# Kernel tuning notes

Hardware: AMD Instinct MI355X
Metric: run time of the kernel (lower is better)

Reference implementation:

```python
import jax, jax.numpy as jnp
import numpy as np

B, IN, HID, OUT = 1024, 512, 128, 64
INP1 = IN + 1  # 513, after prepending ones column


def setup_inputs() -> dict:
    key = jax.random.key(0)
    k1, k2, k3, k4, k5, k6, k7, k8 = jax.random.split(key, 8)
    s1 = 1.0 / np.sqrt(INP1 * INP1)
    s2 = 1.0 / np.sqrt(HID)
    return {
        "img": jax.random.normal(k1, (B, IN), dtype=jnp.float32),
        "tab": jax.random.normal(k2, (B, IN), dtype=jnp.float32),
        "W1": jax.random.uniform(k3, (HID, INP1 * INP1), jnp.float32, -s1, s1),
        "b1": jax.random.uniform(k4, (HID,), jnp.float32, -s1, s1),
        "W2": jax.random.uniform(k5, (HID, HID), jnp.float32, -s2, s2),
        "b2": jax.random.uniform(k6, (HID,), jnp.float32, -s2, s2),
        "W3": jax.random.uniform(k7, (OUT, HID), jnp.float32, -s2, s2),
        "b3": jax.random.uniform(k8, (OUT,), jnp.float32, -s2, s2),
    }


def reference(img, tab, W1, b1, W2, b2, W3, b3):
    ones = jnp.ones((img.shape[0], 1), dtype=img.dtype)
    x = jnp.concatenate([ones, img], axis=1)  # [B, IN+1]
    t = jnp.concatenate([ones, tab], axis=1)  # [B, IN+1]
    # batched outer product, flattened: [B, (IN+1)*(IN+1)]
    fusion = jnp.einsum("bi,bj->bij", x, t).reshape(x.shape[0], -1)
    # dropout is identity in eval mode
    y1 = fusion @ W1.T + b1
    y2 = jnp.tanh(y1 @ W2.T + b2)
    y3 = jax.nn.relu(y2 @ W3.T + b3)
    return y3
```

## Files before the change

### kernel.cpp

```cpp
#include <hip/hip_runtime.h>
#include <hip/hip_bf16.h>

typedef __bf16 bf16x8 __attribute__((ext_vector_type(8)));
typedef float f32x4 __attribute__((ext_vector_type(4)));
typedef float f32x4u __attribute__((ext_vector_type(4), aligned(4)));
typedef unsigned short u16x8 __attribute__((ext_vector_type(8)));

typedef __attribute__((address_space(1))) const unsigned int gu32;
typedef __attribute__((address_space(3))) unsigned int lu32;

#define B_SZ   1024
#define IN_SZ  512
#define HID    128
#define OUT_SZ 64
#define BK     32
#define NKT    16
#define M2     65536

static __device__ __forceinline__ unsigned short f2bf(float f) {
    __hip_bfloat16 h = __float2bfloat16(f);
    return *reinterpret_cast<unsigned short*>(&h);
}

__global__ __launch_bounds__(256) void prep_kernel(
    const float* __restrict__ img, const float* __restrict__ tab,
    unsigned short* __restrict__ tbt, float* __restrict__ xhT,
    float* __restrict__ tc, const float* __restrict__ w1,
    float* __restrict__ wrowT)
{
    const int blk = blockIdx.x;
    for (int j = threadIdx.x; j < 512; j += 256) {
        float v = (j == 0) ? 1.0f : tab[(size_t)blk * IN_SZ + (j - 1)];
        tbt[(size_t)blk * 512 + j] = f2bf(v);
    }
    if (threadIdx.x == 0) tc[blk] = tab[(size_t)blk * IN_SZ + 511];
    if (blk < 513) {
        for (int b = threadIdx.x; b < B_SZ; b += 256)
            xhT[(size_t)blk * B_SZ + b] =
                (blk == 0) ? 1.0f : img[(size_t)b * IN_SZ + (blk - 1)];
    }
    if (blk < 257) {
        const int idx = blk * 256 + threadIdx.x;
        if (idx < 513 * 128) {
            const int j = idx >> 7, h = idx & 127;
            wrowT[idx] = w1[((size_t)h * 513 + 512) * 513 + j];
        }
    }
}

__global__ __launch_bounds__(512, 4) void gemm_fused(
    const float* __restrict__ w1, const unsigned short* __restrict__ tbt,
    const float* __restrict__ xhT, const float* __restrict__ tc,
    float* __restrict__ y1acc)
{
    __shared__ unsigned short Als[3][128 * BK];
    __shared__ unsigned short Bls[3][256 * BK];

    const int wgid = (blockIdx.x & 7) * 256 + (blockIdx.x >> 3);
    const int bm = wgid >> 2;
    const int bn = wgid & 3;
    const int n0 = bn * 256;
    const int h0    = bm >> 2;
    const int ibase = (bm & 3) * 128;
    const int tid  = threadIdx.x;
    const int wv   = tid >> 6;
    const int wr   = wv >> 2;
    const int wc   = wv & 3;
    const int lane = tid & 63;
    const int l15  = lane & 15;
    const int kg   = lane >> 4;

    const int ar  = tid >> 2;
    const int acl = (tid & 3) ^ ((ar >> 1) & 3);
    const float* asrcF = w1 + ((size_t)h0 * 513 + ibase + ar) * 513 + acl * 8;

    const unsigned short* bsrc[2];
    int bBase[2];
    #pragma unroll
    for (int q = 0; q < 2; ++q) {
        const int p  = q * 512 + tid;
        const int r  = p >> 2;
        const int cl = (p & 3) ^ ((r >> 1) & 3);
        bsrc[q] = tbt + (size_t)(n0 + r) * 512 + cl * 8;
        bBase[q] = (q * 512 + wv * 64) * 8;
    }

    int aoffs[4], boffs[4];
    #pragma unroll
    for (int ms = 0; ms < 4; ++ms) {
        const int r = wr * 64 + ms * 16 + l15;
        aoffs[ms] = (r * 4 + (kg ^ ((r >> 1) & 3))) * 8;
    }
    #pragma unroll
    for (int ns = 0; ns < 4; ++ns) {
        const int r = wc * 64 + ns * 16 + l15;
        boffs[ns] = (r * 4 + (kg ^ ((r >> 1) & 3))) * 8;
    }

    f32x4 acc[4][4] = {};
    f32x4u rAlo, rAhi;

#define STB(BUF, KT) do {                                                    \
        const int k32_ = (KT) * BK;                                          \
        _Pragma("unroll")                                                    \
        for (int q_ = 0; q_ < 2; ++q_)                                       \
            __builtin_amdgcn_global_load_lds(                                \
                (gu32*)(const void*)(bsrc[q_] + k32_),                       \
                (lu32*)(void*)&Bls[BUF][bBase[q_]], 16, 0, 0);               \
    } while (0)
#define CVW8(DST, LO, HI) do {                                               \
        u16x8 u_;                                                            \
        u_[0] = f2bf((LO)[0]); u_[1] = f2bf((LO)[1]);                        \
        u_[2] = f2bf((LO)[2]); u_[3] = f2bf((LO)[3]);                        \
        u_[4] = f2bf((HI)[0]); u_[5] = f2bf((HI)[1]);                        \
        u_[6] = f2bf((HI)[2]); u_[7] = f2bf((HI)[3]);                        \
        *reinterpret_cast<u16x8*>(DST) = u_;                                 \
    } while (0)

    {
        const f32x4u t0lo = *reinterpret_cast<const f32x4u*>(asrcF);
        const f32x4u t0hi = *reinterpret_cast<const f32x4u*>(asrcF + 4);
        const f32x4u t1lo = *reinterpret_cast<const f32x4u*>(asrcF + 32);
        const f32x4u t1hi = *reinterpret_cast<const f32x4u*>(asrcF + 36);
        CVW8(&Als[0][tid * 8], t0lo, t0hi);
        CVW8(&Als[1][tid * 8], t1lo, t1hi);
        STB(0, 0);
        STB(1, 1);
    }
    __syncthreads();

    #pragma unroll
    for (int kt = 0; kt < NKT; ++kt) {
        const int cur = kt % 3;
        const unsigned short* ab = &Als[cur][0];
        const unsigned short* bb = &Bls[cur][0];

        if (kt >= 1 && kt + 1 < NKT)
            CVW8(&Als[(kt + 1) % 3][tid * 8], rAlo, rAhi);
        if (kt + 2 < NKT) {
            const float* s_ = asrcF + (kt + 2) * 32;
            rAlo = *reinterpret_cast<const f32x4u*>(s_);
            rAhi = *reinterpret_cast<const f32x4u*>(s_ + 4);
        }

        bf16x8 af[4];
        #pragma unroll
        for (int ms = 0; ms < 4; ++ms)
            af[ms] = *reinterpret_cast<const bf16x8*>(&ab[aoffs[ms]]);
        __builtin_amdgcn_s_setprio(1);
        #pragma unroll
        for (int ns = 0; ns < 4; ++ns) {
            const bf16x8 bf = *reinterpret_cast<const bf16x8*>(&bb[boffs[ns]]);
            #pragma unroll
            for (int ms = 0; ms < 4; ++ms)
                acc[ms][ns] = __builtin_amdgcn_mfma_f32_16x16x32_bf16(
                    af[ms], bf, acc[ms][ns], 0, 0, 0);
        }
        __builtin_amdgcn_s_setprio(0);

        if (kt == NKT - 1) break;

        if (kt + 2 >= NKT) asm volatile("s_waitcnt vmcnt(0)" ::: "memory");
        else               asm volatile("s_waitcnt vmcnt(2)" ::: "memory");
        if (kt + 2 < NKT) STB((kt + 2) % 3, kt + 2);
        asm volatile("s_waitcnt lgkmcnt(0)" ::: "memory");
        __builtin_amdgcn_s_barrier();
        __builtin_amdgcn_sched_barrier(0);
    }
#undef STB
#undef CVW8

    const size_t orow = (size_t)h0 * 513;
    float wcv[4][4];
    #pragma unroll
    for (int ms = 0; ms < 4; ++ms)
        #pragma unroll
        for (int v = 0; v < 4; ++v) {
            const int i_ = ibase + wr * 64 + ms * 16 + kg * 4 + v;
            wcv[ms][v] = w1[(orow + i_) * 513 + 512];
        }

    #pragma unroll
    for (int ns = 0; ns < 4; ++ns) {
        const int ncol = n0 + wc * 64 + ns * 16 + l15;
        const float tv = tc[ncol];
        float s0 = 0.f;
        #pragma unroll
        for (int ms = 0; ms < 4; ++ms) {
            const int i_ = ibase + wr * 64 + ms * 16 + kg * 4;
            #pragma unroll
            for (int v = 0; v < 4; ++v)
                s0 += (acc[ms][ns][v] + wcv[ms][v] * tv)
                      * xhT[(size_t)(i_ + v) * B_SZ + ncol];
        }
        s0 += __shfl_xor(s0, 16); s0 += __shfl_xor(s0, 32);
        if (lane < 16) atomicAdd(&y1acc[(size_t)ncol * HID + h0], s0);
    }
}

__global__ __launch_bounds__(128) void tailmlp_kernel(
    const float* __restrict__ img, const float* __restrict__ tab,
    const float* __restrict__ wrowT, const float* __restrict__ y1acc,
    const float* __restrict__ b1,
    const float* __restrict__ W2, const float* __restrict__ b2,
    const float* __restrict__ W3, const float* __restrict__ b3,
    float* __restrict__ out)
{
    __shared__ float tls[4][513];
    __shared__ float W2p[128][129];
    __shared__ float W3p[64][129];
    __shared__ float y1ls[4][128];
    __shared__ float y2ls[4][128];

    const int b0 = blockIdx.x * 4;
    const int h  = threadIdx.x;

    #pragma unroll
    for (int g = 0; g < 128; ++g) {
        const int idx = g * 128 + h;
        W2p[idx >> 7][idx & 127] = W2[idx];
    }
    #pragma unroll
    for (int g = 0; g < 64; ++g) {
        const int idx = g * 128 + h;
        W3p[idx >> 7][idx & 127] = W3[idx];
    }
    #pragma unroll
    for (int q = 0; q < 4; ++q)
        for (int j = h; j < 513; j += 128)
            tls[q][j] = (j == 0) ? 1.0f : tab[(size_t)(b0 + q) * IN_SZ + (j - 1)];
    __syncthreads();

    {
        float a0 = 0.f, a1 = 0.f, a2 = 0.f, a3 = 0.f;
        #pragma unroll 8
        for (int j = 0; j < 513; ++j) {
            const float w = wrowT[j * 128 + h];
            a0 += w * tls[0][j]; a1 += w * tls[1][j];
            a2 += w * tls[2][j]; a3 += w * tls[3][j];
        }
        const float bb = b1[h];
        y1ls[0][h] = y1acc[(size_t)(b0 + 0) * HID + h] + bb
                     + a0 * img[(size_t)(b0 + 0) * IN_SZ + 511];
        y1ls[1][h] = y1acc[(size_t)(b0 + 1) * HID + h] + bb
                     + a1 * img[(size_t)(b0 + 1) * IN_SZ + 511];
        y1ls[2][h] = y1acc[(size_t)(b0 + 2) * HID + h] + bb
                     + a2 * img[(size_t)(b0 + 2) * IN_SZ + 511];
        y1ls[3][h] = y1acc[(size_t)(b0 + 3) * HID + h] + bb
                     + a3 * img[(size_t)(b0 + 3) * IN_SZ + 511];
    }
    __syncthreads();

    {
        const float bb = b2[h];
        float s[4] = {bb, bb, bb, bb};
        #pragma unroll 16
        for (int k = 0; k < HID; ++k) {
            const float w = W2p[h][k];
            s[0] += w * y1ls[0][k]; s[1] += w * y1ls[1][k];
            s[2] += w * y1ls[2][k]; s[3] += w * y1ls[3][k];
        }
        #pragma unroll
        for (int q = 0; q < 4; ++q) y2ls[q][h] = tanhf(s[q]);
    }
    __syncthreads();

    if (h < OUT_SZ) {
        const float bb = b3[h];
        float s[4] = {bb, bb, bb, bb};
        #pragma unroll 16
        for (int k = 0; k < HID; ++k) {
            const float w = W3p[h][k];
            s[0] += w * y2ls[0][k]; s[1] += w * y2ls[1][k];
            s[2] += w * y2ls[2][k]; s[3] += w * y2ls[3][k];
        }
        #pragma unroll
        for (int q = 0; q < 4; ++q)
            out[(size_t)(b0 + q) * OUT_SZ + h] = fmaxf(s[q], 0.f);
    }
}

__global__ __launch_bounds__(512, 4) void gemm_fused_fb(
    const float* __restrict__ w1, const unsigned short* __restrict__ tbt,
    const float* __restrict__ xhT, const float* __restrict__ tc,
    float* __restrict__ y1acc)
{
    __shared__ float          Afs[2][64 * BK];
    __shared__ unsigned short Bls[2][512 * BK];

    const int bm = blockIdx.x >> 1;
    const int bn = blockIdx.x & 1;
    const int m0 = bm * 64;
    const int n0 = bn * 512;
    const int tid  = threadIdx.x;
    const int wv   = tid >> 6;
    const int lane = tid & 63;
    const int l15  = lane & 15;
    const int kg   = lane >> 4;

    const int ar  = tid >> 3;
    const int acl = (tid & 7) ^ (ar & 7);
    const float* asrc = w1 + (size_t)(m0 + ar) * 513 + acl * 4;
    const int aBase = (wv * 64) * 4;

    const unsigned short* bsrc[4];
    int bBase[4];
    #pragma unroll
    for (int q = 0; q < 4; ++q) {
        const int p  = q * 512 + tid;
        const int r  = p >> 2;
        const int cl = (p & 3) ^ ((r >> 1) & 3);
        bsrc[q] = tbt + (size_t)(n0 + r) * 512 + cl * 8;
        bBase[q] = (q * 512 + wv * 64) * 8;
    }

    int aoff0[4], aoff1[4], boffs[4];
    #pragma unroll
    for (int ms = 0; ms < 4; ++ms) {
        const int r = ms * 16 + l15;
        aoff0[ms] = r * 32 + (((kg * 2) + 0) ^ (r & 7)) * 4;
        aoff1[ms] = r * 32 + (((kg * 2) + 1) ^ (r & 7)) * 4;
    }
    #pragma unroll
    for (int ns = 0; ns < 4; ++ns) {
        const int r = wv * 64 + ns * 16 + l15;
        boffs[ns] = ((r << 2) | (kg ^ ((r >> 1) & 3))) * 8;
    }

    f32x4 acc[4][4] = {};

#define STAGE_FB(BUF, KT) do {                                               \
        const int k32_ = (KT) * BK;                                          \
        _Pragma("unroll")                                                    \
        for (int q_ = 0; q_ < 4; ++q_)                                       \
            __builtin_amdgcn_global_load_lds(                                \
                (gu32*)(const void*)(bsrc[q_] + k32_),                       \
                (lu32*)(void*)&Bls[BUF][bBase[q_]], 16, 0, 0);               \
        __builtin_amdgcn_global_load_lds(                                    \
            (gu32*)(const void*)(asrc + k32_),                               \
            (lu32*)(void*)&Afs[BUF][aBase], 16, 0, 0);                       \
    } while (0)

    STAGE_FB(0, 0);
    __syncthreads();

    for (int kt = 0; kt < NKT; ++kt) {
        const int cur = kt & 1;
        if (kt + 1 < NKT) STAGE_FB(cur ^ 1, kt + 1);

        const float*          ab = &Afs[cur][0];
        const unsigned short* bb = &Bls[cur][0];
        bf16x8 bfr[4];
        #pragma unroll
        for (int ns = 0; ns < 4; ++ns)
            bfr[ns] = *reinterpret_cast<const bf16x8*>(&bb[boffs[ns]]);
        #pragma unroll
        for (int ms = 0; ms < 4; ++ms) {
            const f32x4 lo = *reinterpret_cast<const f32x4*>(&ab[aoff0[ms]]);
            const f32x4 hi = *reinterpret_cast<const f32x4*>(&ab[aoff1[ms]]);
            u16x8 u;
            u[0] = f2bf(lo[0]); u[1] = f2bf(lo[1]);
            u[2] = f2bf(lo[2]); u[3] = f2bf(lo[3]);
            u[4] = f2bf(hi[0]); u[5] = f2bf(hi[1]);
            u[6] = f2bf(hi[2]); u[7] = f2bf(hi[3]);
            const bf16x8 af = __builtin_bit_cast(bf16x8, u);
            #pragma unroll
            for (int ns = 0; ns < 4; ++ns)
                acc[ms][ns] = __builtin_amdgcn_mfma_f32_16x16x32_bf16(
                    af, bfr[ns], acc[ms][ns], 0, 0, 0);
        }
        __syncthreads();
    }
#undef STAGE_FB

    const int h0 = m0 / 513;
    const int mb = (h0 + 1) * 513;
    const bool cross = (mb < m0 + 64);

    float wcv[4][4];
    #pragma unroll
    for (int ms = 0; ms < 4; ++ms)
        #pragma unroll
        for (int v = 0; v < 4; ++v)
            wcv[ms][v] = w1[(size_t)(m0 + ms * 16 + kg * 4 + v) * 513 + 512];

    #pragma unroll
    for (int ns = 0; ns < 4; ++ns) {
        const int ncol = n0 + wv * 64 + ns * 16 + l15;
        const float tv = tc[ncol];
        float s0 = 0.f, s1 = 0.f;
        #pragma unroll
        for (int ms = 0; ms < 4; ++ms) {
            #pragma unroll
            for (int v = 0; v < 4; ++v) {
                const int m = m0 + ms * 16 + kg * 4 + v;
                const bool lo = (m < mb);
                const int i = lo ? (m - h0 * 513) : (m - mb);
                const float val = (acc[ms][ns][v] + wcv[ms][v] * tv)
                                  * xhT[(size_t)i * B_SZ + ncol];
                if (lo) s0 += val; else s1 += val;
            }
        }
        s0 += __shfl_xor(s0, 16); s0 += __shfl_xor(s0, 32);
        if (lane < 16) atomicAdd(&y1acc[(size_t)ncol * HID + h0], s0);
        if (cross) {
            s1 += __shfl_xor(s1, 16); s1 += __shfl_xor(s1, 32);
            if (lane < 16 && (h0 + 1) < HID)
                atomicAdd(&y1acc[(size_t)ncol * HID + h0 + 1], s1);
        }
    }
}

__global__ __launch_bounds__(128) void mlp_kernel(
    const float* __restrict__ y1acc, const float* __restrict__ b1,
    const float* __restrict__ W2, const float* __restrict__ b2,
    const float* __restrict__ W3, const float* __restrict__ b3,
    float* __restrict__ out)
{
    __shared__ float y1r[HID];
    __shared__ float y2r[HID];
    const int b = blockIdx.x;
    const int h = threadIdx.x;
    y1r[h] = y1acc[(size_t)b * HID + h] + b1[h];
    __syncthreads();
    float a = b2[h];
    const float* w2r = W2 + (size_t)h * HID;
    #pragma unroll 8
    for (int k = 0; k < HID; ++k) a += w2r[k] * y1r[k];
    y2r[h] = tanhf(a);
    __syncthreads();
    if (h < OUT_SZ) {
        float a3 = b3[h];
        const float* w3r = W3 + (size_t)h * HID;
        #pragma unroll 8
        for (int k = 0; k < HID; ++k) a3 += w3r[k] * y2r[k];
        out[(size_t)b * OUT_SZ + h] = fmaxf(a3, 0.f);
    }
}

extern "C" void kernel_launch(void* const* d_in, const int* in_sizes, int n_in,
                              void* d_out, int out_size, void* d_ws, size_t ws_size,
                              hipStream_t stream) {
    const float* img = (const float*)d_in[0];
    const float* tab = (const float*)d_in[1];
    const float* W1  = (const float*)d_in[2];
    const float* b1  = (const float*)d_in[3];
    const float* W2  = (const float*)d_in[4];
    const float* b2  = (const float*)d_in[5];
    const float* W3  = (const float*)d_in[6];
    const float* b3  = (const float*)d_in[7];
    float* out = (float*)d_out;

    char* ws = (char*)d_ws;
    float*          y1acc = (float*)ws;
    unsigned short* tbt   = (unsigned short*)(ws + 524288);
    float*          xhT   = (float*)(ws + 1572864);
    float*          tc    = (float*)(ws + 3674112);
    float*          wrowT = (float*)(ws + 3678208);
    const size_t need = 3678208ULL + 262656ULL;

    hipMemsetAsync(y1acc, 0, (size_t)B_SZ * HID * sizeof(float), stream);
    prep_kernel<<<dim3(1024), dim3(256), 0, stream>>>(img, tab, tbt, xhT, tc,
                                                      W1, wrowT);
    if (ws_size >= need) {
        gemm_fused<<<dim3(2048), dim3(512), 0, stream>>>(W1, tbt, xhT, tc, y1acc);
        tailmlp_kernel<<<dim3(256), dim3(128), 0, stream>>>(
            img, tab, wrowT, y1acc, b1, W2, b2, W3, b3, out);
    } else {
        gemm_fused_fb<<<dim3(2052), dim3(512), 0, stream>>>(W1, tbt, xhT, tc, y1acc);
        mlp_kernel<<<dim3(1024), dim3(128), 0, stream>>>(y1acc, b1, W2, b2, W3, b3, out);
    }
}
```

Baseline: 186.4 us.

## Pre-convert W1 to bf16 in prep pass and stream both GEMM operands via LDS DMA

The prep kernel now converts the main block of W1 to a packed bf16 buffer in the workspace. The GEMM then loads both A and B tiles with global_load_lds instead of doing in-loop fp32 loads, bf16 conversion and LDS stores. The GEMM tile shrinks to 128x128 with 256 threads, and the pipeline waits and barriers at the top of each iteration. The aim is to take the conversion and register staging off the MFMA critical path. In exchange there is an extra full pass over W1 that writes a 64 MB intermediate, and the new path needs a much larger workspace, otherwise the fallback runs.

```diff
diff --git a/kernel.cpp b/kernel.cpp
--- a/kernel.cpp
+++ b/kernel.cpp
@@ -24,16 +24,32 @@
 
 __global__ __launch_bounds__(256) void prep_kernel(
     const float* __restrict__ img, const float* __restrict__ tab,
+    const float* __restrict__ w1,
     unsigned short* __restrict__ tbt, float* __restrict__ xhT,
-    float* __restrict__ tc, const float* __restrict__ w1,
-    float* __restrict__ wrowT)
+    float* __restrict__ tc, float* __restrict__ wrowT,
+    unsigned short* __restrict__ w1c)
 {
     const int blk = blockIdx.x;
-    for (int j = threadIdx.x; j < 512; j += 256) {
-        float v = (j == 0) ? 1.0f : tab[(size_t)blk * IN_SZ + (j - 1)];
-        tbt[(size_t)blk * 512 + j] = f2bf(v);
-    }
-    if (threadIdx.x == 0) tc[blk] = tab[(size_t)blk * IN_SZ + 511];
+    {
+        const size_t e = ((size_t)blk * 256 + threadIdx.x) * 8;
+        const int r  = (int)(e >> 9);
+        const int c8 = (int)(e & 511);
+        const size_t srow = (size_t)(r >> 9) * 513 + (r & 511);
+        const float* src = w1 + srow * 513 + c8;
+        const f32x4u lo = *reinterpret_cast<const f32x4u*>(src);
+        const f32x4u hi = *reinterpret_cast<const f32x4u*>(src + 4);
+        u16x8 u;
+        u[0] = f2bf(lo[0]); u[1] = f2bf(lo[1]); u[2] = f2bf(lo[2]); u[3] = f2bf(lo[3]);
+        u[4] = f2bf(hi[0]); u[5] = f2bf(hi[1]); u[6] = f2bf(hi[2]); u[7] = f2bf(hi[3]);
+        *reinterpret_cast<u16x8*>(w1c + (size_t)r * 512 + c8) = u;
+    }
+    if (blk < 1024) {
+        for (int j = threadIdx.x; j < 512; j += 256) {
+            float v = (j == 0) ? 1.0f : tab[(size_t)blk * IN_SZ + (j - 1)];
+            tbt[(size_t)blk * 512 + j] = f2bf(v);
+        }
+        if (threadIdx.x == 0) tc[blk] = tab[(size_t)blk * IN_SZ + 511];
+    }
     if (blk < 513) {
         for (int b = threadIdx.x; b < B_SZ; b += 256)
             xhT[(size_t)blk * B_SZ + b] =
@@ -48,41 +64,41 @@
     }
 }
 
-__global__ __launch_bounds__(512, 4) void gemm_fused(
-    const float* __restrict__ w1, const unsigned short* __restrict__ tbt,
+__global__ __launch_bounds__(256, 3) void gemm_fused(
+    const float* __restrict__ w1, const unsigned short* __restrict__ w1c,
+    const unsigned short* __restrict__ tbt,
     const float* __restrict__ xhT, const float* __restrict__ tc,
     float* __restrict__ y1acc)
 {
     __shared__ unsigned short Als[3][128 * BK];
-    __shared__ unsigned short Bls[3][256 * BK];
-
-    const int wgid = (blockIdx.x & 7) * 256 + (blockIdx.x >> 3);
-    const int bm = wgid >> 2;
-    const int bn = wgid & 3;
-    const int n0 = bn * 256;
+    __shared__ unsigned short Bls[3][128 * BK];
+
+    const int wgid = (blockIdx.x & 7) * 512 + (blockIdx.x >> 3);
+    const int bm = wgid >> 3;
+    const int bn = wgid & 7;
+    const int m0 = bm * 128;
+    const int n0 = bn * 128;
     const int h0    = bm >> 2;
     const int ibase = (bm & 3) * 128;
     const int tid  = threadIdx.x;
     const int wv   = tid >> 6;
-    const int wr   = wv >> 2;
-    const int wc   = wv & 3;
+    const int wr   = wv >> 1;
+    const int wc   = wv & 1;
     const int lane = tid & 63;
     const int l15  = lane & 15;
     const int kg   = lane >> 4;
 
-    const int ar  = tid >> 2;
-    const int acl = (tid & 3) ^ ((ar >> 1) & 3);
-    const float* asrcF = w1 + ((size_t)h0 * 513 + ibase + ar) * 513 + acl * 8;
-
+    const unsigned short* asrc[2];
     const unsigned short* bsrc[2];
-    int bBase[2];
+    int sBase[2];
     #pragma unroll
     for (int q = 0; q < 2; ++q) {
-        const int p  = q * 512 + tid;
+        const int p  = q * 256 + tid;
         const int r  = p >> 2;
         const int cl = (p & 3) ^ ((r >> 1) & 3);
+        asrc[q] = w1c + (size_t)(m0 + r) * 512 + cl * 8;
         bsrc[q] = tbt + (size_t)(n0 + r) * 512 + cl * 8;
-        bBase[q] = (q * 512 + wv * 64) * 8;
+        sBase[q] = (q * 256 + wv * 64) * 8;
     }
 
     int aoffs[4], boffs[4];
@@ -98,77 +114,52 @@
     }
 
     f32x4 acc[4][4] = {};
-    f32x4u rAlo, rAhi;
-
-#define STB(BUF, KT) do {                                                    \
+
+#define STG(BUF, KT) do {                                                    \
         const int k32_ = (KT) * BK;                                          \
         _Pragma("unroll")                                                    \
-        for (int q_ = 0; q_ < 2; ++q_)                                       \
+        for (int q_ = 0; q_ < 2; ++q_) {                                     \
+            __builtin_amdgcn_global_load_lds(                                \
+                (gu32*)(const void*)(asrc[q_] + k32_),                       \
+                (lu32*)(void*)&Als[BUF][sBase[q_]], 16, 0, 0);               \
             __builtin_amdgcn_global_load_lds(                                \
                 (gu32*)(const void*)(bsrc[q_] + k32_),                       \
-                (lu32*)(void*)&Bls[BUF][bBase[q_]], 16, 0, 0);               \
+                (lu32*)(void*)&Bls[BUF][sBase[q_]], 16, 0, 0);               \
+        }                                                                    \
     } while (0)
-#define CVW8(DST, LO, HI) do {                                               \
-        u16x8 u_;                                                            \
-        u_[0] = f2bf((LO)[0]); u_[1] = f2bf((LO)[1]);                        \
-        u_[2] = f2bf((LO)[2]); u_[3] = f2bf((LO)[3]);                        \
-        u_[4] = f2bf((HI)[0]); u_[5] = f2bf((HI)[1]);                        \
-        u_[6] = f2bf((HI)[2]); u_[7] = f2bf((HI)[3]);                        \
-        *reinterpret_cast<u16x8*>(DST) = u_;                                 \
-    } while (0)
-
-    {
-        const f32x4u t0lo = *reinterpret_cast<const f32x4u*>(asrcF);
-        const f32x4u t0hi = *reinterpret_cast<const f32x4u*>(asrcF + 4);
-        const f32x4u t1lo = *reinterpret_cast<const f32x4u*>(asrcF + 32);
-        const f32x4u t1hi = *reinterpret_cast<const f32x4u*>(asrcF + 36);
-        CVW8(&Als[0][tid * 8], t0lo, t0hi);
-        CVW8(&Als[1][tid * 8], t1lo, t1hi);
-        STB(0, 0);
-        STB(1, 1);
-    }
-    __syncthreads();
+
+    STG(0, 0);
+    STG(1, 1);
 
     #pragma unroll
     for (int kt = 0; kt < NKT; ++kt) {
+        if (kt == NKT - 1) asm volatile("s_waitcnt vmcnt(0)" ::: "memory");
+        else               asm volatile("s_waitcnt vmcnt(4)" ::: "memory");
+        __builtin_amdgcn_s_barrier();
+        __builtin_amdgcn_sched_barrier(0);
+
+        if (kt + 2 < NKT) STG((kt + 2) % 3, kt + 2);
+
         const int cur = kt % 3;
         const unsigned short* ab = &Als[cur][0];
         const unsigned short* bb = &Bls[cur][0];
-
-        if (kt >= 1 && kt + 1 < NKT)
-            CVW8(&Als[(kt + 1) % 3][tid * 8], rAlo, rAhi);
-        if (kt + 2 < NKT) {
-            const float* s_ = asrcF + (kt + 2) * 32;
-            rAlo = *reinterpret_cast<const f32x4u*>(s_);
-            rAhi = *reinterpret_cast<const f32x4u*>(s_ + 4);
-        }
-
-        bf16x8 af[4];
+        bf16x8 af[4], bfr[4];
         #pragma unroll
         for (int ms = 0; ms < 4; ++ms)
             af[ms] = *reinterpret_cast<const bf16x8*>(&ab[aoffs[ms]]);
+        #pragma unroll
+        for (int ns = 0; ns < 4; ++ns)
+            bfr[ns] = *reinterpret_cast<const bf16x8*>(&bb[boffs[ns]]);
         __builtin_amdgcn_s_setprio(1);
         #pragma unroll
-        for (int ns = 0; ns < 4; ++ns) {
-            const bf16x8 bf = *reinterpret_cast<const bf16x8*>(&bb[boffs[ns]]);
+        for (int ms = 0; ms < 4; ++ms)
             #pragma unroll
-            for (int ms = 0; ms < 4; ++ms)
+            for (int ns = 0; ns < 4; ++ns)
                 acc[ms][ns] = __builtin_amdgcn_mfma_f32_16x16x32_bf16(
-                    af[ms], bf, acc[ms][ns], 0, 0, 0);
-        }
+                    af[ms], bfr[ns], acc[ms][ns], 0, 0, 0);
         __builtin_amdgcn_s_setprio(0);
-
-        if (kt == NKT - 1) break;
-
-        if (kt + 2 >= NKT) asm volatile("s_waitcnt vmcnt(0)" ::: "memory");
-        else               asm volatile("s_waitcnt vmcnt(2)" ::: "memory");
-        if (kt + 2 < NKT) STB((kt + 2) % 3, kt + 2);
-        asm volatile("s_waitcnt lgkmcnt(0)" ::: "memory");
-        __builtin_amdgcn_s_barrier();
-        __builtin_amdgcn_sched_barrier(0);
-    }
-#undef STB
-#undef CVW8
+    }
+#undef STG
 
     const size_t orow = (size_t)h0 * 513;
     float wcv[4][4];
@@ -411,6 +402,24 @@
     }
 }
 
+__global__ __launch_bounds__(256) void prep_fb_kernel(
+    const float* __restrict__ img, const float* __restrict__ tab,
+    unsigned short* __restrict__ tbt, float* __restrict__ xhT,
+    float* __restrict__ tc)
+{
+    const int blk = blockIdx.x;
+    for (int j = threadIdx.x; j < 512; j += 256) {
+        float v = (j == 0) ? 1.0f : tab[(size_t)blk * IN_SZ + (j - 1)];
+        tbt[(size_t)blk * 512 + j] = f2bf(v);
+    }
+    if (threadIdx.x == 0) tc[blk] = tab[(size_t)blk * IN_SZ + 511];
+    if (blk < 513) {
+        for (int b = threadIdx.x; b < B_SZ; b += 256)
+            xhT[(size_t)blk * B_SZ + b] =
+                (blk == 0) ? 1.0f : img[(size_t)b * IN_SZ + (blk - 1)];
+    }
+}
+
 __global__ __launch_bounds__(128) void mlp_kernel(
     const float* __restrict__ y1acc, const float* __restrict__ b1,
     const float* __restrict__ W2, const float* __restrict__ b2,
@@ -457,16 +466,19 @@
     float*          xhT   = (float*)(ws + 1572864);
     float*          tc    = (float*)(ws + 3674112);
     float*          wrowT = (float*)(ws + 3678208);
-    const size_t need = 3678208ULL + 262656ULL;
+    unsigned short* w1c   = (unsigned short*)(ws + 3940864);
+    const size_t need = 3940864ULL + 67108864ULL;
 
     hipMemsetAsync(y1acc, 0, (size_t)B_SZ * HID * sizeof(float), stream);
-    prep_kernel<<<dim3(1024), dim3(256), 0, stream>>>(img, tab, tbt, xhT, tc,
-                                                      W1, wrowT);
     if (ws_size >= need) {
-        gemm_fused<<<dim3(2048), dim3(512), 0, stream>>>(W1, tbt, xhT, tc, y1acc);
+        prep_kernel<<<dim3(16384), dim3(256), 0, stream>>>(
+            img, tab, W1, tbt, xhT, tc, wrowT, w1c);
+        gemm_fused<<<dim3(4096), dim3(256), 0, stream>>>(
+            W1, w1c, tbt, xhT, tc, y1acc);
         tailmlp_kernel<<<dim3(256), dim3(128), 0, stream>>>(
             img, tab, wrowT, y1acc, b1, W2, b2, W3, b3, out);
     } else {
+        prep_fb_kernel<<<dim3(1024), dim3(256), 0, stream>>>(img, tab, tbt, xhT, tc);
         gemm_fused_fb<<<dim3(2052), dim3(512), 0, stream>>>(W1, tbt, xhT, tc, y1acc);
         mlp_kernel<<<dim3(1024), dim3(128), 0, stream>>>(y1acc, b1, W2, b2, W3, b3, out);
     }
```

Result: slower. 199.1 us (+6.8%).

## Shrink GEMM workgroup tile to 128x128 with 256 threads and 4096 blocks

Applied to the files above, without the earlier changes.

The main fused GEMM now uses a 128x128 output tile with 4 waves in 256-thread workgroups instead of 128x256 with 8 waves, launching twice as many blocks. Each thread now loads and converts two fp32 W1 rows, so the vmcnt threshold is adjusted to match. B fragments are loaded into registers ahead of the MFMA loop rather than interleaved with it. The intent is better occupancy and scheduling, but each W1 tile is now read by twice as many workgroups, which adds global and L2 traffic on the dominant fp32 weight stream.

```diff
diff --git a/kernel.cpp b/kernel.cpp
--- a/kernel.cpp
+++ b/kernel.cpp
@@ -21,8 +21,14 @@
     __hip_bfloat16 h = __float2bfloat16(f);
     return *reinterpret_cast<unsigned short*>(&h);
 }
-
-__global__ __launch_bounds__(256) void prep_kernel(
+static __device__ __forceinline__ u16x8 cv8(f32x4u lo, f32x4u hi) {
+    u16x8 u;
+    u[0] = f2bf(lo[0]); u[1] = f2bf(lo[1]); u[2] = f2bf(lo[2]); u[3] = f2bf(lo[3]);
+    u[4] = f2bf(hi[0]); u[5] = f2bf(hi[1]); u[6] = f2bf(hi[2]); u[7] = f2bf(hi[3]);
+    return u;
+}
+
+__global__ __launch_bounds__(256) void prep_small_kernel(
     const float* __restrict__ img, const float* __restrict__ tab,
     unsigned short* __restrict__ tbt, float* __restrict__ xhT,
     float* __restrict__ tc, const float* __restrict__ w1,
@@ -48,41 +54,41 @@
     }
 }
 
-__global__ __launch_bounds__(512, 4) void gemm_fused(
+__global__ __launch_bounds__(256, 3) void gemm_fused(
     const float* __restrict__ w1, const unsigned short* __restrict__ tbt,
     const float* __restrict__ xhT, const float* __restrict__ tc,
     float* __restrict__ y1acc)
 {
     __shared__ unsigned short Als[3][128 * BK];
-    __shared__ unsigned short Bls[3][256 * BK];
-
-    const int wgid = (blockIdx.x & 7) * 256 + (blockIdx.x >> 3);
-    const int bm = wgid >> 2;
-    const int bn = wgid & 3;
-    const int n0 = bn * 256;
+    __shared__ unsigned short Bls[3][128 * BK];
+
+    const int wgid = (blockIdx.x & 7) * 512 + (blockIdx.x >> 3);
+    const int bm = wgid >> 3;
+    const int bn = wgid & 7;
+    const int n0 = bn * 128;
     const int h0    = bm >> 2;
     const int ibase = (bm & 3) * 128;
     const int tid  = threadIdx.x;
     const int wv   = tid >> 6;
-    const int wr   = wv >> 2;
-    const int wc   = wv & 3;
+    const int wr   = wv >> 1;
+    const int wc   = wv & 1;
     const int lane = tid & 63;
     const int l15  = lane & 15;
     const int kg   = lane >> 4;
 
-    const int ar  = tid >> 2;
-    const int acl = (tid & 3) ^ ((ar >> 1) & 3);
-    const float* asrcF = w1 + ((size_t)h0 * 513 + ibase + ar) * 513 + acl * 8;
-
+    const float* asrcF[2];
+    int aDst[2];
     const unsigned short* bsrc[2];
     int bBase[2];
     #pragma unroll
     for (int q = 0; q < 2; ++q) {
-        const int p  = q * 512 + tid;
+        const int p  = q * 256 + tid;
         const int r  = p >> 2;
         const int cl = (p & 3) ^ ((r >> 1) & 3);
+        asrcF[q] = w1 + ((size_t)h0 * 513 + ibase + r) * 513 + cl * 8;
+        aDst[q]  = p * 8;
         bsrc[q] = tbt + (size_t)(n0 + r) * 512 + cl * 8;
-        bBase[q] = (q * 512 + wv * 64) * 8;
+        bBase[q] = (q * 256 + wv * 64) * 8;
     }
 
     int aoffs[4], boffs[4];
@@ -98,7 +104,7 @@
     }
 
     f32x4 acc[4][4] = {};
-    f32x4u rAlo, rAhi;
+    f32x4u rAlo[2], rAhi[2];
 
 #define STB(BUF, KT) do {                                                    \
         const int k32_ = (KT) * BK;                                          \
@@ -108,22 +114,17 @@
                 (gu32*)(const void*)(bsrc[q_] + k32_),                       \
                 (lu32*)(void*)&Bls[BUF][bBase[q_]], 16, 0, 0);               \
     } while (0)
-#define CVW8(DST, LO, HI) do {                                               \
-        u16x8 u_;                                                            \
-        u_[0] = f2bf((LO)[0]); u_[1] = f2bf((LO)[1]);                        \
-        u_[2] = f2bf((LO)[2]); u_[3] = f2bf((LO)[3]);                        \
-        u_[4] = f2bf((HI)[0]); u_[5] = f2bf((HI)[1]);                        \
-        u_[6] = f2bf((HI)[2]); u_[7] = f2bf((HI)[3]);                        \
-        *reinterpret_cast<u16x8*>(DST) = u_;                                 \
-    } while (0)
 
     {
-        const f32x4u t0lo = *reinterpret_cast<const f32x4u*>(asrcF);
-        const f32x4u t0hi = *reinterpret_cast<const f32x4u*>(asrcF + 4);
-        const f32x4u t1lo = *reinterpret_cast<const f32x4u*>(asrcF + 32);
-        const f32x4u t1hi = *reinterpret_cast<const f32x4u*>(asrcF + 36);
-        CVW8(&Als[0][tid * 8], t0lo, t0hi);
-        CVW8(&Als[1][tid * 8], t1lo, t1hi);
+        #pragma unroll
+        for (int q = 0; q < 2; ++q) {
+            const f32x4u t0lo = *reinterpret_cast<const f32x4u*>(asrcF[q]);
+            const f32x4u t0hi = *reinterpret_cast<const f32x4u*>(asrcF[q] + 4);
+            const f32x4u t1lo = *reinterpret_cast<const f32x4u*>(asrcF[q] + 32);
+            const f32x4u t1hi = *reinterpret_cast<const f32x4u*>(asrcF[q] + 36);
+            *reinterpret_cast<u16x8*>(&Als[0][aDst[q]]) = cv8(t0lo, t0hi);
+            *reinterpret_cast<u16x8*>(&Als[1][aDst[q]]) = cv8(t1lo, t1hi);
+        }
         STB(0, 0);
         STB(1, 1);
     }
@@ -135,40 +136,47 @@
         const unsigned short* ab = &Als[cur][0];
         const unsigned short* bb = &Bls[cur][0];
 
-        if (kt >= 1 && kt + 1 < NKT)
-            CVW8(&Als[(kt + 1) % 3][tid * 8], rAlo, rAhi);
+        if (kt >= 1 && kt + 1 < NKT) {
+            #pragma unroll
+            for (int q = 0; q < 2; ++q)
+                *reinterpret_cast<u16x8*>(&Als[(kt + 1) % 3][aDst[q]]) =
+                    cv8(rAlo[q], rAhi[q]);
+        }
         if (kt + 2 < NKT) {
-            const float* s_ = asrcF + (kt + 2) * 32;
-            rAlo = *reinterpret_cast<const f32x4u*>(s_);
-            rAhi = *reinterpret_cast<const f32x4u*>(s_ + 4);
-        }
-
-        bf16x8 af[4];
+            #pragma unroll
+            for (int q = 0; q < 2; ++q) {
+                const float* s_ = asrcF[q] + (kt + 2) * 32;
+                rAlo[q] = *reinterpret_cast<const f32x4u*>(s_);
+                rAhi[q] = *reinterpret_cast<const f32x4u*>(s_ + 4);
+            }
+        }
+
+        bf16x8 af[4], bfr[4];
         #pragma unroll
         for (int ms = 0; ms < 4; ++ms)
             af[ms] = *reinterpret_cast<const bf16x8*>(&ab[aoffs[ms]]);
+        #pragma unroll
+        for (int ns = 0; ns < 4; ++ns)
+            bfr[ns] = *reinterpret_cast<const bf16x8*>(&bb[boffs[ns]]);
         __builtin_amdgcn_s_setprio(1);
         #pragma unroll
-        for (int ns = 0; ns < 4; ++ns) {
-            const bf16x8 bf = *reinterpret_cast<const bf16x8*>(&bb[boffs[ns]]);
-            #pragma unroll
-            for (int ms = 0; ms < 4; ++ms)
+        for (int ms = 0; ms < 4; ++ms)
+            #pragma unroll
+            for (int ns = 0; ns < 4; ++ns)
                 acc[ms][ns] = __builtin_amdgcn_mfma_f32_16x16x32_bf16(
-                    af[ms], bf, acc[ms][ns], 0, 0, 0);
-        }
+                    af[ms], bfr[ns], acc[ms][ns], 0, 0, 0);
         __builtin_amdgcn_s_setprio(0);
 
         if (kt == NKT - 1) break;
 
         if (kt + 2 >= NKT) asm volatile("s_waitcnt vmcnt(0)" ::: "memory");
-        else               asm volatile("s_waitcnt vmcnt(2)" ::: "memory");
+        else               asm volatile("s_waitcnt vmcnt(4)" ::: "memory");
         if (kt + 2 < NKT) STB((kt + 2) % 3, kt + 2);
         asm volatile("s_waitcnt lgkmcnt(0)" ::: "memory");
         __builtin_amdgcn_s_barrier();
         __builtin_amdgcn_sched_barrier(0);
     }
 #undef STB
-#undef CVW8
 
     const size_t orow = (size_t)h0 * 513;
     float wcv[4][4];
@@ -460,13 +468,16 @@
     const size_t need = 3678208ULL + 262656ULL;
 
     hipMemsetAsync(y1acc, 0, (size_t)B_SZ * HID * sizeof(float), stream);
-    prep_kernel<<<dim3(1024), dim3(256), 0, stream>>>(img, tab, tbt, xhT, tc,
-                                                      W1, wrowT);
     if (ws_size >= need) {
-        gemm_fused<<<dim3(2048), dim3(512), 0, stream>>>(W1, tbt, xhT, tc, y1acc);
+        prep_small_kernel<<<dim3(1024), dim3(256), 0, stream>>>(
+            img, tab, tbt, xhT, tc, W1, wrowT);
+        gemm_fused<<<dim3(4096), dim3(256), 0, stream>>>(
+            W1, tbt, xhT, tc, y1acc);
         tailmlp_kernel<<<dim3(256), dim3(128), 0, stream>>>(
             img, tab, wrowT, y1acc, b1, W2, b2, W3, b3, out);
     } else {
+        prep_small_kernel<<<dim3(1024), dim3(256), 0, stream>>>(
+            img, tab, tbt, xhT, tc, W1, wrowT);
         gemm_fused_fb<<<dim3(2052), dim3(512), 0, stream>>>(W1, tbt, xhT, tc, y1acc);
         mlp_kernel<<<dim3(1024), dim3(128), 0, stream>>>(y1acc, b1, W2, b2, W3, b3, out);
     }
```

Result: slower. 200.4 us (+7.5%).
